# Performance work log

Hardware: AMD Instinct MI355X
Metric: run time of the kernel (lower is better)

Reference implementation:

```python
import jax, jax.numpy as jnp
import numpy as np

N_NODES = 50000
N_EDGES = 300000
D_IN = 256
D_OUT = 256


def setup_inputs() -> dict:
    key = jax.random.key(0)
    k1, k2, k3, k4 = jax.random.split(key, 4)
    x = jax.random.normal(k1, (N_NODES, D_IN), dtype=jnp.float32)
    edge_index = jax.random.randint(k2, (2, N_EDGES), 0, N_NODES, dtype=jnp.int64)
    edge_weight = jax.random.uniform(k3, (N_EDGES,), dtype=jnp.float32)
    # nn.Linear(D_IN, D_OUT, bias=False): weight shape [out, in]
    W = jax.random.normal(k4, (D_OUT, D_IN), dtype=jnp.float32) * (1.0 / np.sqrt(D_IN))
    return {"x": x, "edge_index": edge_index, "edge_weight": edge_weight, "W": W}


def reference(x, edge_index, edge_weight, W):
    # x = self.linear(x)  -> [N, D_OUT]
    x_proj = jnp.einsum("nd,od->no", x, W)
    # torch.sparse.mm(A_hat, x_proj): out[dst] += A[dst, src] * x_proj[src]
    dst = edge_index[0]
    src = edge_index[1]
    msgs = edge_weight[:, None] * x_proj[src]  # [E, D_OUT]
    out = jax.ops.segment_sum(msgs, dst, num_segments=N_NODES)
    return out
```

## Files before the change

kernel.cpp:

```cpp
#include <hip/hip_runtime.h>
#include <stdint.h>

#define D 256

typedef __bf16 bf16x8 __attribute__((ext_vector_type(8)));
typedef unsigned short u16x8 __attribute__((ext_vector_type(8)));
typedef float f32x4 __attribute__((ext_vector_type(4)));

static __device__ inline unsigned short f2bf(float f) {
    union { float f; unsigned u; } c; c.f = f;
    unsigned u = c.u + 0x7FFFu + ((c.u >> 16) & 1u);
    return (unsigned short)(u >> 16);
}
static __device__ inline float bf2f(unsigned short h) {
    union { unsigned u; float f; } c; c.u = (unsigned)h << 16;
    return c.f;
}

__global__ void count_kernel(const int* __restrict__ dst, int* __restrict__ cnt, int E) {
    int e = blockIdx.x * blockDim.x + threadIdx.x;
    if (e < E) atomicAdd(&cnt[dst[e]], 1);
}

__global__ __launch_bounds__(1024) void scan_local_kernel(const int* __restrict__ cnt,
        int* __restrict__ exsc, int* __restrict__ bsum, int n) {
    int t = threadIdx.x;
    int idx = blockIdx.x * 1024 + t;
    int v = (idx < n) ? cnt[idx] : 0;
    __shared__ int tmp[1024];
    tmp[t] = v;
    __syncthreads();
    for (int off = 1; off < 1024; off <<= 1) {
        int u = 0;
        if (t >= off) u = tmp[t - off];
        __syncthreads();
        tmp[t] += u;
        __syncthreads();
    }
    if (idx < n) exsc[idx] = tmp[t] - v;
    if (t == 1023) bsum[blockIdx.x] = tmp[t];
}

__global__ void scan_bsum_kernel(int* __restrict__ bsum, int nb) {
    int t = threadIdx.x;
    int orig = (t < nb) ? bsum[t] : 0;
    int v = orig;
    for (int off = 1; off < 64; off <<= 1) {
        int u = __shfl_up(v, off, 64);
        if (t >= off) v += u;
    }
    if (t < nb) bsum[t] = v - orig;
}

__global__ void finalize_wconv_kernel(const int* __restrict__ exsc, const int* __restrict__ bsum,
        int* __restrict__ offs, int* __restrict__ cur, int n, int E, int finBlocks,
        const float* __restrict__ Wp, unsigned short* __restrict__ Wbf) {
    if ((int)blockIdx.x >= finBlocks) {
        int f = ((int)blockIdx.x - finBlocks) * 256 + threadIdx.x;
        if (f < 8192) {
            int nr = f >> 5;
            int k0 = (f & 31) << 3;
            const float4* p = (const float4*)(Wp + (size_t)nr * D + k0);
            float4 v0 = p[0], v1 = p[1];
            u16x8 h;
            h[0] = f2bf(v0.x); h[1] = f2bf(v0.y); h[2] = f2bf(v0.z); h[3] = f2bf(v0.w);
            h[4] = f2bf(v1.x); h[5] = f2bf(v1.y); h[6] = f2bf(v1.z); h[7] = f2bf(v1.w);
            int t = nr >> 4, l16 = nr & 15;
            int s = k0 >> 5, q = (k0 >> 3) & 3;
            ((u16x8*)Wbf)[(t * 8 + s) * 64 + q * 16 + l16] = h;
        }
        return;
    }
    int idx = (int)blockIdx.x * 256 + threadIdx.x;
    if (idx < n) {
        int o = exsc[idx] + bsum[idx >> 10];
        offs[idx] = o;
        cur[idx]  = o;
    }
    if (idx == 0) offs[n] = E;
}

__global__ __launch_bounds__(256, 3) void gemm3_kernel(
        const float* __restrict__ X, const unsigned short* __restrict__ Wbf,
        unsigned short* __restrict__ xproj, int M, int gemmBlocks,
        const int* __restrict__ dst, const int* __restrict__ src,
        const float* __restrict__ ew, int* __restrict__ cur,
        uint2* __restrict__ pairS, int E) {
    __shared__ u16x8 Asm[32 * 64];

    int tid = threadIdx.x;

    if ((int)blockIdx.x >= gemmBlocks) {
        int e = ((int)blockIdx.x - gemmBlocks) * 256 + tid;
        if (e < E) {
            int d = dst[e];
            int pos = atomicAdd(&cur[d], 1);
            uint2 pk;
            pk.x = (unsigned)src[e];
            pk.y = __float_as_uint(ew[e]);
            pairS[pos] = pk;
        }
        return;
    }

    int m0  = (int)blockIdx.x * 64;
    int row = tid >> 2, akc = tid & 3;
    int grow = m0 + row; if (grow > M - 1) grow = M - 1;
    const float* ab = X + (size_t)grow * D + akc * 8;

#pragma unroll
    for (int s = 0; s < 8; ++s) {
        const float4* p = (const float4*)(ab + s * 32);
        float4 v0 = p[0], v1 = p[1];
        u16x8 h;
        h[0] = f2bf(v0.x); h[1] = f2bf(v0.y); h[2] = f2bf(v0.z); h[3] = f2bf(v0.w);
        h[4] = f2bf(v1.x); h[5] = f2bf(v1.y); h[6] = f2bf(v1.z); h[7] = f2bf(v1.w);
        Asm[(s * 4 + akc) * 64 + row] = h;
    }
    __syncthreads();

    int lane = tid & 63, wn = tid >> 6;
    int l16 = lane & 15, lq = lane >> 4;

    f32x4 acc[4][4];
#pragma unroll
    for (int i = 0; i < 4; ++i)
#pragma unroll
        for (int j = 0; j < 4; ++j)
            acc[i][j] = (f32x4){0.f, 0.f, 0.f, 0.f};

    const u16x8* wbp = (const u16x8*)Wbf + (size_t)(wn * 32) * 64 + lane;
    u16x8 bcur[4];
#pragma unroll
    for (int fn = 0; fn < 4; ++fn) bcur[fn] = wbp[(fn * 8) * 64];

#pragma unroll
    for (int s = 0; s < 8; ++s) {
        u16x8 bnx[4];
#pragma unroll
        for (int fn = 0; fn < 4; ++fn)
            bnx[fn] = wbp[(fn * 8 + ((s + 1) & 7)) * 64];
        u16x8 af[4];
#pragma unroll
        for (int fm = 0; fm < 4; ++fm)
            af[fm] = Asm[(s * 4 + lq) * 64 + fm * 16 + l16];
#pragma unroll
        for (int fm = 0; fm < 4; ++fm)
#pragma unroll
            for (int fn = 0; fn < 4; ++fn)
                acc[fm][fn] = __builtin_amdgcn_mfma_f32_16x16x32_bf16(
                    __builtin_bit_cast(bf16x8, af[fm]),
                    __builtin_bit_cast(bf16x8, bcur[fn]),
                    acc[fm][fn], 0, 0, 0);
#pragma unroll
        for (int fn = 0; fn < 4; ++fn) bcur[fn] = bnx[fn];
    }

    __syncthreads();
    unsigned short* Ls = (unsigned short*)Asm;
#pragma unroll
    for (int fm = 0; fm < 4; ++fm) {
        int r0 = fm * 16 + lq * 4;
#pragma unroll
        for (int fn = 0; fn < 4; ++fn) {
            int cs = (wn * 64 + fn * 16 + l16) ^ (lq << 4);
#pragma unroll
            for (int r = 0; r < 4; ++r)
                Ls[(r0 + r) * 256 + cs] = f2bf(acc[fm][fn][r]);
        }
    }
    __syncthreads();
    const u16x8* Lv = (const u16x8*)Asm;
#pragma unroll
    for (int it = 0; it < 8; ++it) {
        int slot = it * 256 + tid;
        int rr = slot >> 5, c8 = slot & 31;
        int idx = rr * 32 + (c8 ^ (((rr >> 2) & 3) << 1));
        int orow = m0 + rr;
        if (orow < M)
            ((u16x8*)(xproj + (size_t)orow * D))[c8] = Lv[idx];
    }
}

__global__ __launch_bounds__(512) void aggp_kernel(const ushort4* __restrict__ P,
        const int* __restrict__ offs, const uint2* __restrict__ pairS,
        float4* __restrict__ out4, int N) {
    int wave = threadIdx.x >> 6;
    int lane = threadIdx.x & 63;
    int node = blockIdx.x * 8 + wave;
    if (node >= N) return;
    int beg = offs[node], end = offs[node + 1];
    float ax = 0.f, ay = 0.f, az = 0.f, aw = 0.f;
    int e = beg;
    for (; e + 3 < end; e += 4) {
        uint2 p0 = pairS[e],     p1 = pairS[e + 1];
        uint2 p2 = pairS[e + 2], p3 = pairS[e + 3];
        float w0 = __uint_as_float(p0.y), w1 = __uint_as_float(p1.y);
        float w2 = __uint_as_float(p2.y), w3 = __uint_as_float(p3.y);
        ushort4 h0 = P[(size_t)p0.x * 64 + lane];
        ushort4 h1 = P[(size_t)p1.x * 64 + lane];
        ushort4 h2 = P[(size_t)p2.x * 64 + lane];
        ushort4 h3 = P[(size_t)p3.x * 64 + lane];
        ax += w0 * bf2f(h0.x); ay += w0 * bf2f(h0.y); az += w0 * bf2f(h0.z); aw += w0 * bf2f(h0.w);
        ax += w1 * bf2f(h1.x); ay += w1 * bf2f(h1.y); az += w1 * bf2f(h1.z); aw += w1 * bf2f(h1.w);
        ax += w2 * bf2f(h2.x); ay += w2 * bf2f(h2.y); az += w2 * bf2f(h2.z); aw += w2 * bf2f(h2.w);
        ax += w3 * bf2f(h3.x); ay += w3 * bf2f(h3.y); az += w3 * bf2f(h3.z); aw += w3 * bf2f(h3.w);
    }
    for (; e < end; ++e) {
        uint2 p0 = pairS[e];
        float w0 = __uint_as_float(p0.y);
        ushort4 h0 = P[(size_t)p0.x * 64 + lane];
        ax += w0 * bf2f(h0.x); ay += w0 * bf2f(h0.y); az += w0 * bf2f(h0.z); aw += w0 * bf2f(h0.w);
    }
    float4 r; r.x = ax; r.y = ay; r.z = az; r.w = aw;
    out4[(size_t)node * 64 + lane] = r;
}

__global__ void scan_finalize_kernel(const int* __restrict__ exsc, const int* __restrict__ bsum,
        int* __restrict__ offs, int* __restrict__ cur, int n, int E) {
    int idx = blockIdx.x * blockDim.x + threadIdx.x;
    if (idx < n) {
        int o = exsc[idx] + bsum[idx >> 10];
        offs[idx] = o;
        cur[idx]  = o;
    }
    if (idx == 0) offs[n] = E;
}

__global__ void fill_kernel(const int* __restrict__ dst, const int* __restrict__ src,
        const float* __restrict__ ew, int* __restrict__ cur,
        int* __restrict__ srcS, float* __restrict__ wS, int E) {
    int e = blockIdx.x * blockDim.x + threadIdx.x;
    if (e < E) {
        int d = dst[e];
        int pos = atomicAdd(&cur[d], 1);
        srcS[pos] = src[e];
        wS[pos]   = ew[e];
    }
}

__global__ __launch_bounds__(256) void agg_kernel(const float4* __restrict__ X4,
        const int* __restrict__ offs, const int* __restrict__ srcS,
        const float* __restrict__ wS, float4* __restrict__ agg4, int N) {
    int wave = threadIdx.x >> 6;
    int lane = threadIdx.x & 63;
    int node = blockIdx.x * 4 + wave;
    if (node >= N) return;
    int beg = offs[node], end = offs[node + 1];
    float ax = 0.f, ay = 0.f, az = 0.f, aw = 0.f;
    for (int e = beg; e < end; ++e) {
        int sN = srcS[e];
        float wt = wS[e];
        float4 xv = X4[(size_t)sN * 64 + lane];
        ax += wt * xv.x; ay += wt * xv.y; az += wt * xv.z; aw += wt * xv.w;
    }
    float4 r; r.x = ax; r.y = ay; r.z = az; r.w = aw;
    agg4[(size_t)node * 64 + lane] = r;
}

__global__ __launch_bounds__(256) void gemm_kernel(const float* __restrict__ A,
        const float* __restrict__ Wp, float* __restrict__ out, int M) {
    __shared__ u16x8 Asm[4 * 64];
    __shared__ u16x8 Bsm[4 * 256];
    int tid  = threadIdx.x;
    int lane = tid & 63;
    int wn   = tid >> 6;
    int m0   = blockIdx.x * 64;
    f32x4 acc[4][4];
#pragma unroll
    for (int i = 0; i < 4; ++i)
#pragma unroll
        for (int j = 0; j < 4; ++j)
            acc[i][j] = (f32x4){0.f, 0.f, 0.f, 0.f};
    int arow = tid >> 2;
    int akc  = tid & 3;
    int grow = m0 + arow; if (grow > M - 1) grow = M - 1;
    const float* aBase = A + (size_t)grow * D + akc * 8;
    int l16 = lane & 15, lq = lane >> 4;
    for (int s = 0; s < 8; ++s) {
        int k0 = s * 32;
        {
            const float4* p = (const float4*)(aBase + k0);
            float4 v0 = p[0], v1 = p[1];
            u16x8 h;
            h[0] = f2bf(v0.x); h[1] = f2bf(v0.y); h[2] = f2bf(v0.z); h[3] = f2bf(v0.w);
            h[4] = f2bf(v1.x); h[5] = f2bf(v1.y); h[6] = f2bf(v1.z); h[7] = f2bf(v1.w);
            Asm[akc * 64 + arow] = h;
        }
#pragma unroll
        for (int j = 0; j < 4; ++j) {
            int n = j * 64 + (tid >> 2);
            const float4* p = (const float4*)(Wp + (size_t)n * D + k0 + akc * 8);
            float4 v0 = p[0], v1 = p[1];
            u16x8 h;
            h[0] = f2bf(v0.x); h[1] = f2bf(v0.y); h[2] = f2bf(v0.z); h[3] = f2bf(v0.w);
            h[4] = f2bf(v1.x); h[5] = f2bf(v1.y); h[6] = f2bf(v1.z); h[7] = f2bf(v1.w);
            Bsm[akc * 256 + n] = h;
        }
        __syncthreads();
        u16x8 af[4], bfr[4];
#pragma unroll
        for (int fm = 0; fm < 4; ++fm) af[fm] = Asm[lq * 64 + fm * 16 + l16];
#pragma unroll
        for (int fn = 0; fn < 4; ++fn) bfr[fn] = Bsm[lq * 256 + wn * 64 + fn * 16 + l16];
#pragma unroll
        for (int fm = 0; fm < 4; ++fm)
#pragma unroll
            for (int fn = 0; fn < 4; ++fn)
                acc[fm][fn] = __builtin_amdgcn_mfma_f32_16x16x32_bf16(
                    __builtin_bit_cast(bf16x8, af[fm]),
                    __builtin_bit_cast(bf16x8, bfr[fn]),
                    acc[fm][fn], 0, 0, 0);
        __syncthreads();
    }
#pragma unroll
    for (int fm = 0; fm < 4; ++fm)
#pragma unroll
        for (int fn = 0; fn < 4; ++fn)
#pragma unroll
            for (int r = 0; r < 4; ++r) {
                int row = m0 + fm * 16 + lq * 4 + r;
                int col = wn * 64 + fn * 16 + l16;
                if (row < M) out[(size_t)row * D + col] = acc[fm][fn][r];
            }
}

extern "C" void kernel_launch(void* const* d_in, const int* in_sizes, int n_in,
                              void* d_out, int out_size, void* d_ws, size_t ws_size,
                              hipStream_t stream) {
    const float* X  = (const float*)d_in[0];
    const int*   ei = (const int*)d_in[1];
    const float* ew = (const float*)d_in[2];
    const float* Wp = (const float*)d_in[3];
    float* out = (float*)d_out;

    int N = in_sizes[0] / D;
    int E = in_sizes[2];
    const int* dst = ei;
    const int* src = ei + E;
    int nb = (N + 1023) / 1024;

    size_t xpBytes  = (size_t)N * D * sizeof(unsigned short);
    size_t wbBytes  = (size_t)D * D * sizeof(unsigned short);
    size_t csrInts  = (size_t)4 * N + 1 + nb + 2 * (size_t)E;
    size_t csrBytes = csrInts * sizeof(int);
    bool planB = (ws_size >= xpBytes + wbBytes + csrBytes + 512);

    uint8_t* ws = (uint8_t*)d_ws;
    unsigned short* xproj = (unsigned short*)ws;
    unsigned short* Wbf = (unsigned short*)(ws + ((xpBytes + 255) & ~(size_t)255));
    int* csr = planB ? (int*)((uint8_t*)Wbf + ((wbBytes + 255) & ~(size_t)255)) : (int*)ws;

    int* cnt  = csr;
    int* offs = cnt + N;
    int* cur  = offs + N + 1;
    int* edg  = cur + N;
    uint2* pairS = (uint2*)edg;
    int* srcS = edg;
    float* wS = (float*)(srcS + E);
    int* exsc = (int*)(edg + 2 * (size_t)E);
    int* bsum = exsc + N;

    hipMemsetAsync(cnt, 0, (size_t)N * sizeof(int), stream);
    count_kernel<<<dim3((E + 255) / 256), dim3(256), 0, stream>>>(dst, cnt, E);
    scan_local_kernel<<<dim3(nb), dim3(1024), 0, stream>>>(cnt, exsc, bsum, N);
    scan_bsum_kernel<<<dim3(1), dim3(64), 0, stream>>>(bsum, nb);

    if (planB) {
        int finBlocks = (N + 255) / 256;
        finalize_wconv_kernel<<<dim3(finBlocks + 32), dim3(256), 0, stream>>>(
            exsc, bsum, offs, cur, N, E, finBlocks, Wp, Wbf);
        int gemmBlocks = (N + 63) / 64;
        int fillBlocks = (E + 255) / 256;
        gemm3_kernel<<<dim3(gemmBlocks + fillBlocks), dim3(256), 0, stream>>>(
            X, Wbf, xproj, N, gemmBlocks, dst, src, ew, cur, pairS, E);
        aggp_kernel<<<dim3((N + 7) / 8), dim3(512), 0, stream>>>(
            (const ushort4*)xproj, offs, pairS, (float4*)out, N);
    } else {
        scan_finalize_kernel<<<dim3((N + 255) / 256), dim3(256), 0, stream>>>(exsc, bsum, offs, cur, N, E);
        fill_kernel<<<dim3((E + 255) / 256), dim3(256), 0, stream>>>(dst, src, ew, cur, srcS, wS, E);
        agg_kernel<<<dim3((N + 3) / 4), dim3(256), 0, stream>>>((const float4*)X, offs, srcS, wS,
                                                                (float4*)out, N);
        gemm_kernel<<<dim3((N + 63) / 64), dim3(256), 0, stream>>>(out, Wp, out, N);
    }
}
```

Before: 169.7 us.

## Record per-edge rank during count and fuse count into GEMM launch

The count atomics now run inside the GEMM launch and store each edge's rank, so the CSR fill needs no second atomic pass. The memset is replaced by a zeroing kernel that also converts W to bf16. The fill becomes a deterministic scatter fused with offset finalization. This removes launches and atomic contention, at the cost of an extra rank array (E ints) to write and read, which changes the workspace layout and can push the code onto the fallback path.

```diff
diff --git a/kernel.cpp b/kernel.cpp
--- a/kernel.cpp
+++ b/kernel.cpp
@@ -17,9 +17,122 @@
     return c.f;
 }
 
-__global__ void count_kernel(const int* __restrict__ dst, int* __restrict__ cnt, int E) {
-    int e = blockIdx.x * blockDim.x + threadIdx.x;
-    if (e < E) atomicAdd(&cnt[dst[e]], 1);
+__global__ void zero_wconv_kernel(int* __restrict__ cnt, int n, int zBlocks,
+        const float* __restrict__ Wp, unsigned short* __restrict__ Wbf) {
+    if ((int)blockIdx.x < zBlocks) {
+        int i = (int)blockIdx.x * 256 + threadIdx.x;
+        if (i < n) cnt[i] = 0;
+        return;
+    }
+    int f = ((int)blockIdx.x - zBlocks) * 256 + threadIdx.x;
+    if (f < 8192) {
+        int nr = f >> 5;
+        int k0 = (f & 31) << 3;
+        const float4* p = (const float4*)(Wp + (size_t)nr * D + k0);
+        float4 v0 = p[0], v1 = p[1];
+        u16x8 h;
+        h[0] = f2bf(v0.x); h[1] = f2bf(v0.y); h[2] = f2bf(v0.z); h[3] = f2bf(v0.w);
+        h[4] = f2bf(v1.x); h[5] = f2bf(v1.y); h[6] = f2bf(v1.z); h[7] = f2bf(v1.w);
+        int t = nr >> 4, l16 = nr & 15;
+        int s = k0 >> 5, q = (k0 >> 3) & 3;
+        ((u16x8*)Wbf)[(t * 8 + s) * 64 + q * 16 + l16] = h;
+    }
+}
+
+__global__ __launch_bounds__(256, 3) void gemm_count_kernel(
+        const float* __restrict__ X, const unsigned short* __restrict__ Wbf,
+        unsigned short* __restrict__ xproj, int M, int gemmBlocks,
+        const int* __restrict__ dst, int* __restrict__ cnt, int* __restrict__ rank, int E) {
+    __shared__ u16x8 Asm[32 * 64];
+
+    int tid = threadIdx.x;
+
+    if ((int)blockIdx.x >= gemmBlocks) {
+        int e = ((int)blockIdx.x - gemmBlocks) * 256 + tid;
+        if (e < E) {
+            int d = dst[e];
+            rank[e] = atomicAdd(&cnt[d], 1);
+        }
+        return;
+    }
+
+    int m0  = (int)blockIdx.x * 64;
+    int row = tid >> 2, akc = tid & 3;
+    int grow = m0 + row; if (grow > M - 1) grow = M - 1;
+    const float* ab = X + (size_t)grow * D + akc * 8;
+
+#pragma unroll
+    for (int s = 0; s < 8; ++s) {
+        const float4* p = (const float4*)(ab + s * 32);
+        float4 v0 = p[0], v1 = p[1];
+        u16x8 h;
+        h[0] = f2bf(v0.x); h[1] = f2bf(v0.y); h[2] = f2bf(v0.z); h[3] = f2bf(v0.w);
+        h[4] = f2bf(v1.x); h[5] = f2bf(v1.y); h[6] = f2bf(v1.z); h[7] = f2bf(v1.w);
+        Asm[(s * 4 + akc) * 64 + row] = h;
+    }
+    __syncthreads();
+
+    int lane = tid & 63, wn = tid >> 6;
+    int l16 = lane & 15, lq = lane >> 4;
+
+    f32x4 acc[4][4];
+#pragma unroll
+    for (int i = 0; i < 4; ++i)
+#pragma unroll
+        for (int j = 0; j < 4; ++j)
+            acc[i][j] = (f32x4){0.f, 0.f, 0.f, 0.f};
+
+    const u16x8* wbp = (const u16x8*)Wbf + (size_t)(wn * 32) * 64 + lane;
+    u16x8 bcur[4];
+#pragma unroll
+    for (int fn = 0; fn < 4; ++fn) bcur[fn] = wbp[(fn * 8) * 64];
+
+#pragma unroll
+    for (int s = 0; s < 8; ++s) {
+        u16x8 bnx[4];
+#pragma unroll
+        for (int fn = 0; fn < 4; ++fn)
+            bnx[fn] = wbp[(fn * 8 + ((s + 1) & 7)) * 64];
+        u16x8 af[4];
+#pragma unroll
+        for (int fm = 0; fm < 4; ++fm)
+            af[fm] = Asm[(s * 4 + lq) * 64 + fm * 16 + l16];
+#pragma unroll
+        for (int fm = 0; fm < 4; ++fm)
+#pragma unroll
+            for (int fn = 0; fn < 4; ++fn)
+                acc[fm][fn] = __builtin_amdgcn_mfma_f32_16x16x32_bf16(
+                    __builtin_bit_cast(bf16x8, af[fm]),
+                    __builtin_bit_cast(bf16x8, bcur[fn]),
+                    acc[fm][fn], 0, 0, 0);
+#pragma unroll
+        for (int fn = 0; fn < 4; ++fn) bcur[fn] = bnx[fn];
+    }
+
+    __syncthreads();
+    unsigned short* Ls = (unsigned short*)Asm;
+#pragma unroll
+    for (int fm = 0; fm < 4; ++fm) {
+        int r0 = fm * 16 + lq * 4;
+#pragma unroll
+        for (int fn = 0; fn < 4; ++fn) {
+            int cs = (wn * 64 + fn * 16 + l16) ^ (lq << 4);
+#pragma unroll
+            for (int r = 0; r < 4; ++r)
+                Ls[(r0 + r) * 256 + cs] = f2bf(acc[fm][fn][r]);
+        }
+    }
+    __syncthreads();
+    const u16x8* Lv = (const u16x8*)Asm;
+#pragma unroll
+    for (int it = 0; it < 8; ++it) {
+        int slot = it * 256 + tid;
+        int rr = slot >> 5, c8 = slot & 31;
+        int idx = rr * 32 + (c8 ^ (((rr >> 2) & 3) << 1));
+        int orow = m0 + rr;
+        if (orow < M)
+            ((u16x8*)(xproj + (size_t)orow * D))[c8] = Lv[idx];
+    }
 }
 
 __global__ __launch_bounds__(1024) void scan_local_kernel(const int* __restrict__ cnt,
@@ -52,133 +165,25 @@
     if (t < nb) bsum[t] = v - orig;
 }
 
-__global__ void finalize_wconv_kernel(const int* __restrict__ exsc, const int* __restrict__ bsum,
-        int* __restrict__ offs, int* __restrict__ cur, int n, int E, int finBlocks,
-        const float* __restrict__ Wp, unsigned short* __restrict__ Wbf) {
-    if ((int)blockIdx.x >= finBlocks) {
-        int f = ((int)blockIdx.x - finBlocks) * 256 + threadIdx.x;
-        if (f < 8192) {
-            int nr = f >> 5;
-            int k0 = (f & 31) << 3;
-            const float4* p = (const float4*)(Wp + (size_t)nr * D + k0);
-            float4 v0 = p[0], v1 = p[1];
-            u16x8 h;
-            h[0] = f2bf(v0.x); h[1] = f2bf(v0.y); h[2] = f2bf(v0.z); h[3] = f2bf(v0.w);
-            h[4] = f2bf(v1.x); h[5] = f2bf(v1.y); h[6] = f2bf(v1.z); h[7] = f2bf(v1.w);
-            int t = nr >> 4, l16 = nr & 15;
-            int s = k0 >> 5, q = (k0 >> 3) & 3;
-            ((u16x8*)Wbf)[(t * 8 + s) * 64 + q * 16 + l16] = h;
-        }
+__global__ void finalize_fill_kernel(const int* __restrict__ exsc, const int* __restrict__ bsum,
+        int* __restrict__ offs, int n, int E, int finBlocks,
+        const int* __restrict__ dst, const int* __restrict__ src,
+        const float* __restrict__ ew, const int* __restrict__ rank,
+        uint2* __restrict__ pairS) {
+    if ((int)blockIdx.x < finBlocks) {
+        int idx = (int)blockIdx.x * 256 + threadIdx.x;
+        if (idx < n) offs[idx] = exsc[idx] + bsum[idx >> 10];
+        if (idx == 0) offs[n] = E;
         return;
     }
-    int idx = (int)blockIdx.x * 256 + threadIdx.x;
-    if (idx < n) {
-        int o = exsc[idx] + bsum[idx >> 10];
-        offs[idx] = o;
-        cur[idx]  = o;
-    }
-    if (idx == 0) offs[n] = E;
-}
-
-__global__ __launch_bounds__(256, 3) void gemm3_kernel(
-        const float* __restrict__ X, const unsigned short* __restrict__ Wbf,
-        unsigned short* __restrict__ xproj, int M, int gemmBlocks,
-        const int* __restrict__ dst, const int* __restrict__ src,
-        const float* __restrict__ ew, int* __restrict__ cur,
-        uint2* __restrict__ pairS, int E) {
-    __shared__ u16x8 Asm[32 * 64];
-
-    int tid = threadIdx.x;
-
-    if ((int)blockIdx.x >= gemmBlocks) {
-        int e = ((int)blockIdx.x - gemmBlocks) * 256 + tid;
-        if (e < E) {
-            int d = dst[e];
-            int pos = atomicAdd(&cur[d], 1);
-            uint2 pk;
-            pk.x = (unsigned)src[e];
-            pk.y = __float_as_uint(ew[e]);
-            pairS[pos] = pk;
-        }
-        return;
-    }
-
-    int m0  = (int)blockIdx.x * 64;
-    int row = tid >> 2, akc = tid & 3;
-    int grow = m0 + row; if (grow > M - 1) grow = M - 1;
-    const float* ab = X + (size_t)grow * D + akc * 8;
-
-#pragma unroll
-    for (int s = 0; s < 8; ++s) {
-        const float4* p = (const float4*)(ab + s * 32);
-        float4 v0 = p[0], v1 = p[1];
-        u16x8 h;
-        h[0] = f2bf(v0.x); h[1] = f2bf(v0.y); h[2] = f2bf(v0.z); h[3] = f2bf(v0.w);
-        h[4] = f2bf(v1.x); h[5] = f2bf(v1.y); h[6] = f2bf(v1.z); h[7] = f2bf(v1.w);
-        Asm[(s * 4 + akc) * 64 + row] = h;
-    }
-    __syncthreads();
-
-    int lane = tid & 63, wn = tid >> 6;
-    int l16 = lane & 15, lq = lane >> 4;
-
-    f32x4 acc[4][4];
-#pragma unroll
-    for (int i = 0; i < 4; ++i)
-#pragma unroll
-        for (int j = 0; j < 4; ++j)
-            acc[i][j] = (f32x4){0.f, 0.f, 0.f, 0.f};
-
-    const u16x8* wbp = (const u16x8*)Wbf + (size_t)(wn * 32) * 64 + lane;
-    u16x8 bcur[4];
-#pragma unroll
-    for (int fn = 0; fn < 4; ++fn) bcur[fn] = wbp[(fn * 8) * 64];
-
-#pragma unroll
-    for (int s = 0; s < 8; ++s) {
-        u16x8 bnx[4];
-#pragma unroll
-        for (int fn = 0; fn < 4; ++fn)
-            bnx[fn] = wbp[(fn * 8 + ((s + 1) & 7)) * 64];
-        u16x8 af[4];
-#pragma unroll
-        for (int fm = 0; fm < 4; ++fm)
-            af[fm] = Asm[(s * 4 + lq) * 64 + fm * 16 + l16];
-#pragma unroll
-        for (int fm = 0; fm < 4; ++fm)
-#pragma unroll
-            for (int fn = 0; fn < 4; ++fn)
-                acc[fm][fn] = __builtin_amdgcn_mfma_f32_16x16x32_bf16(
-                    __builtin_bit_cast(bf16x8, af[fm]),
-                    __builtin_bit_cast(bf16x8, bcur[fn]),
-                    acc[fm][fn], 0, 0, 0);
-#pragma unroll
-        for (int fn = 0; fn < 4; ++fn) bcur[fn] = bnx[fn];
-    }
-
-    __syncthreads();
-    unsigned short* Ls = (unsigned short*)Asm;
-#pragma unroll
-    for (int fm = 0; fm < 4; ++fm) {
-        int r0 = fm * 16 + lq * 4;
-#pragma unroll
-        for (int fn = 0; fn < 4; ++fn) {
-            int cs = (wn * 64 + fn * 16 + l16) ^ (lq << 4);
-#pragma unroll
-            for (int r = 0; r < 4; ++r)
-                Ls[(r0 + r) * 256 + cs] = f2bf(acc[fm][fn][r]);
-        }
-    }
-    __syncthreads();
-    const u16x8* Lv = (const u16x8*)Asm;
-#pragma unroll
-    for (int it = 0; it < 8; ++it) {
-        int slot = it * 256 + tid;
-        int rr = slot >> 5, c8 = slot & 31;
-        int idx = rr * 32 + (c8 ^ (((rr >> 2) & 3) << 1));
-        int orow = m0 + rr;
-        if (orow < M)
-            ((u16x8*)(xproj + (size_t)orow * D))[c8] = Lv[idx];
+    int e = ((int)blockIdx.x - finBlocks) * 256 + threadIdx.x;
+    if (e < E) {
+        int d = dst[e];
+        int pos = exsc[d] + bsum[d >> 10] + rank[e];
+        uint2 pk;
+        pk.x = (unsigned)src[e];
+        pk.y = __float_as_uint(ew[e]);
+        pairS[pos] = pk;
     }
 }
 
@@ -216,6 +221,11 @@
     out4[(size_t)node * 64 + lane] = r;
 }
 
+__global__ void count_kernel(const int* __restrict__ dst, int* __restrict__ cnt, int E) {
+    int e = blockIdx.x * blockDim.x + threadIdx.x;
+    if (e < E) atomicAdd(&cnt[dst[e]], 1);
+}
+
 __global__ void scan_finalize_kernel(const int* __restrict__ exsc, const int* __restrict__ bsum,
         int* __restrict__ offs, int* __restrict__ cur, int n, int E) {
     int idx = blockIdx.x * blockDim.x + threadIdx.x;
@@ -342,41 +352,53 @@
 
     size_t xpBytes  = (size_t)N * D * sizeof(unsigned short);
     size_t wbBytes  = (size_t)D * D * sizeof(unsigned short);
-    size_t csrInts  = (size_t)4 * N + 1 + nb + 2 * (size_t)E;
-    size_t csrBytes = csrInts * sizeof(int);
-    bool planB = (ws_size >= xpBytes + wbBytes + csrBytes + 512);
+    size_t intCnt   = 2 * (size_t)E + (size_t)E + 3 * (size_t)N + 1 + nb;
+    size_t intBytes = intCnt * sizeof(int);
+    bool planB = (ws_size >= xpBytes + wbBytes + intBytes + 512);
 
     uint8_t* ws = (uint8_t*)d_ws;
     unsigned short* xproj = (unsigned short*)ws;
     unsigned short* Wbf = (unsigned short*)(ws + ((xpBytes + 255) & ~(size_t)255));
-    int* csr = planB ? (int*)((uint8_t*)Wbf + ((wbBytes + 255) & ~(size_t)255)) : (int*)ws;
-
-    int* cnt  = csr;
-    int* offs = cnt + N;
-    int* cur  = offs + N + 1;
-    int* edg  = cur + N;
-    uint2* pairS = (uint2*)edg;
-    int* srcS = edg;
-    float* wS = (float*)(srcS + E);
-    int* exsc = (int*)(edg + 2 * (size_t)E);
-    int* bsum = exsc + N;
-
-    hipMemsetAsync(cnt, 0, (size_t)N * sizeof(int), stream);
-    count_kernel<<<dim3((E + 255) / 256), dim3(256), 0, stream>>>(dst, cnt, E);
-    scan_local_kernel<<<dim3(nb), dim3(1024), 0, stream>>>(cnt, exsc, bsum, N);
-    scan_bsum_kernel<<<dim3(1), dim3(64), 0, stream>>>(bsum, nb);
+    int* ib = (int*)((uint8_t*)Wbf + ((wbBytes + 255) & ~(size_t)255));
 
     if (planB) {
+        uint2* pairS = (uint2*)ib;
+        int* rank = ib + 2 * (size_t)E;
+        int* cnt  = rank + E;
+        int* offs = cnt + N;
+        int* exsc = offs + N + 1;
+        int* bsum = exsc + N;
+
+        int zBlocks = (N + 255) / 256;
+        zero_wconv_kernel<<<dim3(zBlocks + 32), dim3(256), 0, stream>>>(cnt, N, zBlocks, Wp, Wbf);
+
+        int gemmBlocks  = (N + 63) / 64;
+        int countBlocks = (E + 255) / 256;
+        gemm_count_kernel<<<dim3(gemmBlocks + countBlocks), dim3(256), 0, stream>>>(
+            X, Wbf, xproj, N, gemmBlocks, dst, cnt, rank, E);
+
+        scan_local_kernel<<<dim3(nb), dim3(1024), 0, stream>>>(cnt, exsc, bsum, N);
+        scan_bsum_kernel<<<dim3(1), dim3(64), 0, stream>>>(bsum, nb);
+
         int finBlocks = (N + 255) / 256;
-        finalize_wconv_kernel<<<dim3(finBlocks + 32), dim3(256), 0, stream>>>(
-            exsc, bsum, offs, cur, N, E, finBlocks, Wp, Wbf);
-        int gemmBlocks = (N + 63) / 64;
-        int fillBlocks = (E + 255) / 256;
-        gemm3_kernel<<<dim3(gemmBlocks + fillBlocks), dim3(256), 0, stream>>>(
-            X, Wbf, xproj, N, gemmBlocks, dst, src, ew, cur, pairS, E);
+        finalize_fill_kernel<<<dim3(finBlocks + countBlocks), dim3(256), 0, stream>>>(
+            exsc, bsum, offs, N, E, finBlocks, dst, src, ew, rank, pairS);
+
         aggp_kernel<<<dim3((N + 7) / 8), dim3(512), 0, stream>>>(
             (const ushort4*)xproj, offs, pairS, (float4*)out, N);
     } else {
+        int* cnt  = ib;
+        int* offs = cnt + N;
+        int* cur  = offs + N + 1;
+        int* srcS = cur + N;
+        float* wS = (float*)(srcS + E);
+        int* exsc = (int*)(wS + E);
+        int* bsum = exsc + N;
+
+        hipMemsetAsync(cnt, 0, (size_t)N * sizeof(int), stream);
+        count_kernel<<<dim3((E + 255) / 256), dim3(256), 0, stream>>>(dst, cnt, E);
+        scan_local_kernel<<<dim3(nb), dim3(1024), 0, stream>>>(cnt, exsc, bsum, N);
+        scan_bsum_kernel<<<dim3(1), dim3(64), 0, stream>>>(bsum, nb);
         scan_finalize_kernel<<<dim3((N + 255) / 256), dim3(256), 0, stream>>>(exsc, bsum, offs, cur, N, E);
         fill_kernel<<<dim3((E + 255) / 256), dim3(256), 0, stream>>>(dst, src, ew, cur, srcS, wS, E);
         agg_kernel<<<dim3((N + 3) / 4), dim3(256), 0, stream>>>((const float4*)X, offs, srcS, wS,
```

After: 164.2 us. 3.2% less time.
